# Kernel tuning notes

Measured on AMD Instinct MI355X. Metric: run time of the kernel, lower is better.

## Reference

```python
import jax, jax.numpy as jnp
import numpy as np

B, C_IN, FH, TW = 64, 8, 128, 128
FBINS, A, M_ARR, M_SRC = 257, 360, 4, 2
EPS = 1e-6


def _conv2d(x, w):
    return jax.lax.conv_general_dilated(x, w, (1, 1), 'SAME', dimension_numbers=('NCHW', 'OIHW', 'NCHW'))


def _bn(x, g, b, m, v):
    sh = (1, -1, 1, 1)
    return (x - m.reshape(sh)) * jax.lax.rsqrt(v.reshape(sh) + 1e-5) * g.reshape(sh) + b.reshape(sh)


def _pool2(x):
    b_, c, h, w = x.shape
    return x.reshape(b_, c, h // 2, 2, w // 2, 2).max(axis=(3, 5))


def _block(x, w, g, b, m, v):
    return _pool2(jax.nn.relu(_bn(_conv2d(x, w), g, b, m, v)))


def _conv1d(x, w, b):
    return jax.lax.conv_general_dilated(x, w, (1,), 'SAME', dimension_numbers=('NCH', 'OIH', 'NCH')) + b[None, :, None]


def setup_inputs() -> dict:
    ks = jax.random.split(jax.random.key(0), 16)
    r = lambda i, shp, s=1.0: jax.random.normal(ks[i], shp, dtype=jnp.float32) * s
    d = {
        'X': r(0, (B, C_IN, FH, TW)),
        'sv_real': r(1, (B, FBINS, A, M_ARR)),
        'sv_imag': r(2, (B, FBINS, A, M_ARR)),
        'correlation': jnp.zeros((1,), jnp.float32),
        'conv1_w': r(3, (64, C_IN, 3, 3), 0.1),
        'conv2_w': r(4, (64, 64, 3, 3), 0.04),
        'conv3_w': r(5, (64, 64, 3, 3), 0.04),
        'conv4_w': r(6, (FBINS, 64, 3, 3), 0.04),
        'fc_w': r(7, (32, 64), 0.1),
        'fc_b': jnp.zeros((32,), jnp.float32),
        'convs2_w': r(8, (FBINS, FBINS, 3), 0.02),
        'convs2_b': jnp.zeros((FBINS,), jnp.float32),
        'convs1_w': r(9, (1, FBINS, 3), 0.03),
        'convs1_b': jnp.zeros((1,), jnp.float32),
        'ca_w1': r(10, (16, FBINS), 0.06),
        'ca_w2': r(11, (FBINS, 16), 0.2),
    }
    for i, c in [(1, 64), (2, 64), (3, 64), (4, FBINS)]:
        d[f'bn{i}_g'] = jnp.ones((c,), jnp.float32)
        d[f'bn{i}_b'] = jnp.zeros((c,), jnp.float32)
        d[f'bn{i}_m'] = jnp.zeros((c,), jnp.float32)
        d[f'bn{i}_v'] = jnp.ones((c,), jnp.float32)
    return d


def reference(X, sv_real, sv_imag, correlation,
              conv1_w, bn1_g, bn1_b, bn1_m, bn1_v,
              conv2_w, bn2_g, bn2_b, bn2_m, bn2_v,
              conv3_w, bn3_g, bn3_b, bn3_m, bn3_v,
              conv4_w, bn4_g, bn4_b, bn4_m, bn4_v,
              fc_w, fc_b, convs2_w, convs2_b, convs1_w, convs1_b,
              ca_w1, ca_w2):
    b_ = X.shape[0]
    # CNN encoder: (B,8,128,128) -> (B,257,8,8)
    z = _block(X, conv1_w, bn1_g, bn1_b, bn1_m, bn1_v)
    z = _block(z, conv2_w, bn2_g, bn2_b, bn2_m, bn2_v)
    z = _block(z, conv3_w, bn3_g, bn3_b, bn3_m, bn3_v)
    z = _block(z, conv4_w, bn4_g, bn4_b, bn4_m, bn4_v)
    z = z.reshape(b_, FBINS, -1) @ fc_w.T + fc_b            # (B,257,32)
    z = z.reshape(b_, FBINS, C_IN // 2, C_IN)               # (B,257,4,8)
    Rz = jax.lax.complex(z[..., :M_ARR], z[..., M_ARR:])    # (B,257,4,4)
    # hermitianize + diagonal loading
    Rz = 0.5 * (Rz + jnp.conj(jnp.swapaxes(Rz, -1, -2)))
    Rz = Rz + 1e-5 * jnp.eye(M_ARR, dtype=Rz.dtype)
    _, evecs = jnp.linalg.eigh(Rz)                          # ascending eigenvalues
    Un = evecs[..., ::-1][..., M_SRC:]                      # noise subspace (B,F,4,2)
    UnUnH = Un @ jnp.conj(jnp.swapaxes(Un, -1, -2))         # (B,F,4,4)
    svc = jnp.conj(jax.lax.complex(sv_real, sv_imag))       # (B,F,A,4)
    # faithful to torch code: denom[a] = sum_{m,n} conj(sv[a,m]) UnUnH[m,n] conj(sv[a,n])
    denom = jnp.real(jnp.einsum('bfam,bfmn,bfan->bfa', svc, UnUnH, svc))
    spectrum = 1.0 / jnp.maximum(denom, EPS)                # (B,257,360)
    spectrum = jax.nn.leaky_relu(_conv1d(spectrum, convs2_w, convs2_b), 0.1)
    # channel attention over the 257 freq channels
    y = spectrum.mean(-1)                                   # (B,257)
    att = jax.nn.sigmoid(jax.nn.relu(y @ ca_w1.T) @ ca_w2.T)
    spectrum = spectrum * att[:, :, None]
    spectrum = jax.nn.sigmoid(_conv1d(spectrum, convs1_w, convs1_b))[:, 0, :]  # (B,360)
    # soft-argmax over top-5 peaks
    angles = jnp.linspace(0.0, 360.0, A + 1)[:-1]
    vals, idx = jax.lax.top_k(spectrum, 5)
    wts = jax.nn.softmax(20.0 * vals, axis=-1)
    doa = (wts * angles[idx]).sum(-1)[:, None]              # (B,1)
    return doa, spectrum
```

## Files before the change

kernel.cpp:

```cpp
#include <hip/hip_runtime.h>

typedef unsigned short u16;
typedef unsigned int u32;
typedef short short8 __attribute__((ext_vector_type(8)));
typedef float f32x4 __attribute__((ext_vector_type(4)));

#define NB 64
#define NFB 257
#define NANG 360

__device__ __forceinline__ u16 f2bf(float x) {
    u32 u = __float_as_uint(x);
    u = (u + 0x7fffu + ((u >> 16) & 1u)) >> 16;
    return (u16)u;
}
__device__ __forceinline__ float bf2f(u16 h) { return __uint_as_float(((u32)h) << 16); }

__global__ __launch_bounds__(256) void bnprep(
    const float* g1, const float* b1, const float* m1, const float* v1,
    const float* g2, const float* b2, const float* m2, const float* v2,
    const float* g3, const float* b3, const float* m3, const float* v3,
    const float* g4, const float* b4, const float* m4, const float* v4,
    float* out)
{
    int L = blockIdx.x;
    const float* gs[4] = {g1, g2, g3, g4};
    const float* bs[4] = {b1, b2, b3, b4};
    const float* ms[4] = {m1, m2, m3, m4};
    const float* vs[4] = {v1, v2, v3, v4};
    int n = (L == 3) ? 257 : 64;
    float* sc = out + L * 1024;
    float* bi = sc + 512;
    for (int i = threadIdx.x; i < n; i += 256) {
        float s = gs[L][i] * rsqrtf(vs[L][i] + 1e-5f);
        sc[i] = s;
        bi[i] = bs[L][i] - ms[L][i] * s;
    }
}

__global__ __launch_bounds__(256) void bpack(
    const float* __restrict__ w, u16* __restrict__ Bp,
    int CREAL, int OCREAL, int NT, int KCC, int NFTOT)
{
    int i = blockIdx.x * 256 + threadIdx.x;
    int total = NT * KCC * 2 * NFTOT * 64;
    if (i >= total) return;
    int lane = i & 63;
    int t = i >> 6;
    int nf = t % NFTOT;
    int th = t / NFTOT;
    int h = th & 1;
    int chunk = th >> 1;
    int s = chunk / KCC, kc = chunk % KCC;
    int n = nf * 16 + (lane & 15);
    int k0 = kc * 32 + (lane >> 4) * 8;
    u16 o8[8];
    #pragma unroll
    for (int e = 0; e < 8; ++e) {
        int k = k0 + e;
        float v = 0.f;
        if (k < CREAL && n < OCREAL) v = w[((size_t)n * CREAL + k) * NT + s];
        u16 hh = f2bf(v);
        o8[e] = (h == 0) ? hh : f2bf(v - bf2f(hh));
    }
    u16* d = Bp + (size_t)i * 8;
    #pragma unroll
    for (int e = 0; e < 8; ++e) d[e] = o8[e];
}

__global__ __launch_bounds__(256) void bpack1(const float* __restrict__ w, u16* __restrict__ Bp)
{
    int i = blockIdx.x * 256 + threadIdx.x;
    if (i >= 3 * 2 * 4 * 64) return;
    int lane = i & 63;
    int t = i >> 6;
    int nf = t % 4;
    int th = t / 4;
    int h = th & 1;
    int ky = th >> 1;
    int n = nf * 16 + (lane & 15);
    int q = lane >> 4;
    u16 o8[8];
    #pragma unroll
    for (int e = 0; e < 8; ++e) {
        float v = (q < 3) ? w[((size_t)(n * 8 + e) * 3 + ky) * 3 + q] : 0.f;
        u16 hh = f2bf(v);
        o8[e] = (h == 0) ? hh : f2bf(v - bf2f(hh));
    }
    u16* d = Bp + (size_t)i * 8;
    #pragma unroll
    for (int e = 0; e < 8; ++e) d[e] = o8[e];
}

__global__ __launch_bounds__(256) void xpack_kernel(
    const float* __restrict__ X, u16* __restrict__ hi, u16* __restrict__ lo)
{
    __shared__ float Xs[8][132];
    int bid = blockIdx.x;
    int prow = bid % 130;
    int b = bid / 130;
    bool inr = (prow >= 1 && prow <= 128);
    for (int i = threadIdx.x; i < 8 * 130; i += 256) {
        int c = i / 130, pcol = i % 130;
        float v = 0.f;
        if (inr && pcol >= 1 && pcol <= 128)
            v = X[(((size_t)b * 8 + c) * 128 + (prow - 1)) * 128 + (pcol - 1)];
        Xs[c][pcol] = v;
    }
    __syncthreads();
    for (int p = threadIdx.x; p < 130; p += 256) {
        short8 h8, l8;
        #pragma unroll
        for (int c = 0; c < 8; ++c) {
            float f = Xs[c][p];
            u16 hh = f2bf(f);
            h8[c] = (short)hh;
            l8[c] = (short)f2bf(f - bf2f(hh));
        }
        size_t o = (((size_t)b * 130 + prow) * 130 + p) * 8;
        *(short8*)(hi + o) = h8;
        *(short8*)(lo + o) = l8;
    }
}

__global__ __launch_bounds__(256) void zpad(
    u16* hi, u16* lo, int Bn, int Hp, int Wp, int Cb, int doCols)
{
    int perB = 2 * Wp + (doCols ? 2 * (Hp - 2) : 0);
    long total = (long)Bn * perB * Cb;
    for (long idx = blockIdx.x * 256L + threadIdx.x; idx < total; idx += (long)gridDim.x * 256) {
        int c = (int)(idx % Cb);
        long t = idx / Cb;
        int p = (int)(t % perB);
        int b = (int)(t / perB);
        int row, col;
        if (p < Wp) { row = 0; col = p; }
        else if (p < 2 * Wp) { row = Hp - 1; col = p - Wp; }
        else { int pp = p - 2 * Wp; row = 1 + (pp >> 1); col = (pp & 1) ? (Wp - 1) : 0; }
        size_t o = (((size_t)b * Hp + row) * Wp + col) * Cb + c;
        hi[o] = 0;
        lo[o] = 0;
    }
}

__global__ __launch_bounds__(256) void conv_c1(
    const u16* __restrict__ Ahi, const u16* __restrict__ Alo,
    const u16* __restrict__ Bp,
    const float* __restrict__ esc, const float* __restrict__ ebi,
    u16* __restrict__ Ohi, u16* __restrict__ Olo)
{
    constexpr int Wst = 130, Hp = 130;
    constexpr int SROWS = 5;
    constexpr int SPIX = SROWS * Wst;
    constexpr int STAGEB = SPIX * 16;
    __shared__ __align__(16) char sm[2 * STAGEB];

    int bid = blockIdx.x;
    int ytile = bid % 64;
    int b = bid / 64;
    int y0 = ytile * 2;
    int tid = threadIdx.x;
    int wv = tid >> 6;
    int l = tid & 63;
    int r = l & 15, q = l >> 4;

    for (int pix = tid; pix < SPIX; pix += 256) {
        int prow = y0 + pix / Wst, pcol = pix % Wst;
        uint4 vh = {0, 0, 0, 0}, vl = {0, 0, 0, 0};
        if (prow < Hp) {
            size_t g = (((size_t)b * Hp + prow) * Wst + pcol) * 16;
            vh = *(const uint4*)((const char*)Ahi + g);
            vl = *(const uint4*)((const char*)Alo + g);
        }
        *(uint4*)(sm + pix * 16) = vh;
        *(uint4*)(sm + STAGEB + pix * 16) = vl;
    }
    __syncthreads();

    f32x4 acc[4][4] = {};

    #pragma unroll
    for (int ky = 0; ky < 3; ++ky) {
        short8 bh[4], bl[4];
        #pragma unroll
        for (int ni = 0; ni < 4; ++ni) {
            const u16* bt = Bp + ((size_t)(ky * 2) * 4 + ni) * 512 + l * 8;
            bh[ni] = *(const short8*)bt;
            bl[ni] = *(const short8*)(bt + 4 * 512);
        }
        short8 ah[4], al[4];
        #pragma unroll
        for (int mi = 0; mi < 4; ++mi) {
            int pf = wv * 2 + (mi >> 1);
            int y = mi & 1;
            int p = (y + ky) * Wst + pf * 16 + r + q;
            ah[mi] = *(const short8*)(sm + p * 16);
            al[mi] = *(const short8*)(sm + STAGEB + p * 16);
        }
        #pragma unroll
        for (int ni = 0; ni < 4; ++ni)
            #pragma unroll
            for (int mi = 0; mi < 4; ++mi) {
                acc[mi][ni] = __builtin_amdgcn_mfma_f32_16x16x32_bf16(ah[mi], bh[ni], acc[mi][ni], 0, 0, 0);
                acc[mi][ni] = __builtin_amdgcn_mfma_f32_16x16x32_bf16(ah[mi], bl[ni], acc[mi][ni], 0, 0, 0);
                acc[mi][ni] = __builtin_amdgcn_mfma_f32_16x16x32_bf16(al[mi], bh[ni], acc[mi][ni], 0, 0, 0);
            }
    }

    #pragma unroll
    for (int ni = 0; ni < 4; ++ni) {
        int oc = ni * 16 + r;
        float sc0 = esc[oc], bi0 = ebi[oc];
        #pragma unroll
        for (int pi = 0; pi < 2; ++pi) {
            int pf = wv * 2 + pi;
            #pragma unroll
            for (int k = 0; k < 2; ++k) {
                float m = -3.4e38f;
                #pragma unroll
                for (int dmi = 0; dmi < 2; ++dmi)
                    #pragma unroll
                    for (int dj = 0; dj < 2; ++dj)
                        m = fmaxf(m, fmaf(acc[2 * pi + dmi][ni][2 * k + dj], sc0, bi0));
                m = fmaxf(m, 0.f);
                int x2 = pf * 8 + q * 2 + k;
                size_t o = (((size_t)b * 66 + (y0 / 2 + 1)) * 66 + (x2 + 1)) * 64 + oc;
                u16 hh = f2bf(m);
                Ohi[o] = hh;
                Olo[o] = f2bf(m - bf2f(hh));
            }
        }
    }
}

template<int H, int W, int OC, int R, int NF, int MFW, int OUTMODE, int NFTOT>
__global__ __launch_bounds__(256) void conv_gemm(
    const u16* __restrict__ Ahi, const u16* __restrict__ Alo,
    const u16* __restrict__ Bp,
    const float* __restrict__ esc, const float* __restrict__ ebi,
    u16* __restrict__ Ohi, u16* __restrict__ Olo, float* __restrict__ Of)
{
    constexpr int Wst = W + 2, Hp = H + 2;
    constexpr int SROWS = R + 2;
    constexpr int SPIX = SROWS * Wst;
    constexpr int XF = W / 16;
    constexpr int STAGEB = SPIX * 64;
    constexpr int HT = H / R;
    __shared__ __align__(16) char sm[2 * STAGEB];

    int bid = blockIdx.x;
    int ytile = bid % HT;
    int b = bid / HT;
    int tid = threadIdx.x;
    int wv = tid >> 6;
    int l = tid & 63;
    int r = l & 15, q = l >> 4;
    int y0 = ytile * R;
    int nfg0 = blockIdx.y * NF;

    f32x4 acc[MFW][NF] = {};
    short8 Bh[2][NF], Bl[2][NF];

    auto loadB = [&](int buf, int chunk) {
        #pragma unroll
        for (int ni = 0; ni < NF; ++ni) {
            const u16* bt = Bp + ((size_t)(chunk * 2) * NFTOT + nfg0 + ni) * 512 + l * 8;
            Bh[buf][ni] = *(const short8*)bt;
            Bl[buf][ni] = *(const short8*)(bt + (size_t)NFTOT * 512);
        }
    };
    loadB(0, 0);

    #pragma unroll
    for (int cs = 0; cs < 2; ++cs) {
        __syncthreads();
        for (int i = tid; i < SPIX * 4; i += 256) {
            int pix = i >> 2, sub = i & 3;
            int prow = y0 + pix / Wst, pcol = pix % Wst;
            uint4 vh = {0, 0, 0, 0}, vl = {0, 0, 0, 0};
            if (prow < Hp) {
                size_t g = (((size_t)b * Hp + prow) * Wst + pcol) * 128 + cs * 64 + sub * 16;
                vh = *(const uint4*)((const char*)Ahi + g);
                vl = *(const uint4*)((const char*)Alo + g);
            }
            int dst = (pix << 6) + ((sub ^ ((pix >> 1) & 3)) << 4);
            *(uint4*)(sm + dst) = vh;
            *(uint4*)(sm + STAGEB + dst) = vl;
        }
        __syncthreads();

        #pragma unroll
        for (int s = 0; s < 9; ++s) {
            int cur = (cs * 9 + s) & 1;
            if (s < 8) loadB(cur ^ 1, (s + 1) * 2 + cs);
            else if (cs == 0) loadB(cur ^ 1, 1);
            int ky = s / 3, kx = s % 3;
            short8 ah[MFW], al[MFW];
            #pragma unroll
            for (int mi = 0; mi < MFW; ++mi) {
                int pf = wv * (MFW / 2) + (mi >> 1);
                int y = (pf / XF) * 2 + (mi & 1);
                int xf = pf % XF;
                int p = (y + ky) * Wst + xf * 16 + kx + r;
                int off = (p << 6) + ((q ^ ((p >> 1) & 3)) << 4);
                ah[mi] = *(const short8*)(sm + off);
                al[mi] = *(const short8*)(sm + STAGEB + off);
            }
            #pragma unroll
            for (int ni = 0; ni < NF; ++ni)
                #pragma unroll
                for (int mi = 0; mi < MFW; ++mi) {
                    acc[mi][ni] = __builtin_amdgcn_mfma_f32_16x16x32_bf16(ah[mi], Bh[cur][ni], acc[mi][ni], 0, 0, 0);
                    acc[mi][ni] = __builtin_amdgcn_mfma_f32_16x16x32_bf16(ah[mi], Bl[cur][ni], acc[mi][ni], 0, 0, 0);
                    acc[mi][ni] = __builtin_amdgcn_mfma_f32_16x16x32_bf16(al[mi], Bh[cur][ni], acc[mi][ni], 0, 0, 0);
                }
        }
    }

    #pragma unroll
    for (int ni = 0; ni < NF; ++ni) {
        int oc = (nfg0 + ni) * 16 + r;
        float sc0 = esc[oc], bi0 = ebi[oc];
        #pragma unroll
        for (int pi = 0; pi < MFW / 2; ++pi) {
            int pf = wv * (MFW / 2) + pi;
            int y2 = y0 / 2 + pf / XF;
            int xb = (pf % XF) * 8 + q * 2;
            #pragma unroll
            for (int k = 0; k < 2; ++k) {
                float m = -3.4e38f;
                #pragma unroll
                for (int dmi = 0; dmi < 2; ++dmi)
                    #pragma unroll
                    for (int dj = 0; dj < 2; ++dj)
                        m = fmaxf(m, fmaf(acc[2 * pi + dmi][ni][2 * k + dj], sc0, bi0));
                m = fmaxf(m, 0.f);
                int x2 = xb + k;
                if (OUTMODE == 0) {
                    size_t o = (((size_t)b * (H / 2 + 2) + y2 + 1) * (W / 2 + 2) + (x2 + 1)) * 64 + oc;
                    u16 hh = f2bf(m);
                    Ohi[o] = hh;
                    Olo[o] = f2bf(m - bf2f(hh));
                } else {
                    if (oc < OC)
                        Of[(((size_t)b * (H / 2) + y2) * (W / 2) + x2) * (size_t)OC + oc] = m;
                }
            }
        }
    }
}

__global__ __launch_bounds__(512) void convs2_gemm(
    const u16* __restrict__ Ahi, const u16* __restrict__ Alo,
    const u16* __restrict__ Bp, const float* __restrict__ bia,
    float* __restrict__ sp2)
{
    constexpr int SPIX = 386;
    constexpr int STAGEB = SPIX * 64;
    __shared__ __align__(16) char sm[2 * STAGEB];

    int b = blockIdx.x;
    int nt = blockIdx.y;
    int tid = threadIdx.x;
    int wv = tid >> 6;
    int l = tid & 63;
    int r = l & 15, q = l >> 4;

    f32x4 acc[3][3] = {};
    short8 Bh[2][3], Bl[2][3];

    auto loadB = [&](int buf, int chunk) {
        #pragma unroll
        for (int ni = 0; ni < 3; ++ni) {
            const u16* bt = Bp + ((size_t)(chunk * 2) * 18 + nt * 3 + ni) * 512 + l * 8;
            Bh[buf][ni] = *(const short8*)bt;
            Bl[buf][ni] = *(const short8*)(bt + 18 * 512);
        }
    };
    loadB(0, 0);

    #pragma unroll
    for (int cs = 0; cs < 9; ++cs) {
        __syncthreads();
        for (int i = tid; i < SPIX * 4; i += 512) {
            int pix = i >> 2, sub = i & 3;
            uint4 vh = {0, 0, 0, 0}, vl = {0, 0, 0, 0};
            if (pix < 362) {
                size_t g = ((size_t)b * 362 + pix) * 576 + (size_t)cs * 64 + (size_t)sub * 16;
                vh = *(const uint4*)((const char*)Ahi + g);
                vl = *(const uint4*)((const char*)Alo + g);
            }
            int dst = (pix << 6) + ((sub ^ ((pix >> 1) & 3)) << 4);
            *(uint4*)(sm + dst) = vh;
            *(uint4*)(sm + STAGEB + dst) = vl;
        }
        __syncthreads();

        #pragma unroll
        for (int ky = 0; ky < 3; ++ky) {
            int cur = (cs * 3 + ky) & 1;
            if (ky < 2) loadB(cur ^ 1, (ky + 1) * 9 + cs);
            else if (cs < 8) loadB(cur ^ 1, cs + 1);
            #pragma unroll
            for (int mi = 0; mi < 3; ++mi) {
                int p = (wv * 3 + mi) * 16 + r + ky;
                int off = (p << 6) + ((q ^ ((p >> 1) & 3)) << 4);
                short8 ah = *(const short8*)(sm + off);
                short8 al = *(const short8*)(sm + STAGEB + off);
                #pragma unroll
                for (int ni = 0; ni < 3; ++ni) {
                    acc[mi][ni] = __builtin_amdgcn_mfma_f32_16x16x32_bf16(ah, Bh[cur][ni], acc[mi][ni], 0, 0, 0);
                    acc[mi][ni] = __builtin_amdgcn_mfma_f32_16x16x32_bf16(ah, Bl[cur][ni], acc[mi][ni], 0, 0, 0);
                    acc[mi][ni] = __builtin_amdgcn_mfma_f32_16x16x32_bf16(al, Bh[cur][ni], acc[mi][ni], 0, 0, 0);
                }
            }
        }
    }

    #pragma unroll
    for (int ni = 0; ni < 3; ++ni) {
        int n = (nt * 3 + ni) * 16 + r;
        if (n >= NFB) continue;
        float bi0 = bia[n];
        #pragma unroll
        for (int mi = 0; mi < 3; ++mi) {
            int t0 = (wv * 3 + mi) * 16 + q * 4;
            #pragma unroll
            for (int j = 0; j < 4; ++j) {
                int t = t0 + j;
                if (t < NANG) {
                    float v = acc[mi][ni][j] + bi0;
                    sp2[((size_t)b * NANG + t) * NFB + n] = (v >= 0.f) ? v : 0.1f * v;
                }
            }
        }
    }
}

__global__ __launch_bounds__(256) void fc_kernel(
    const float* __restrict__ z, const float* __restrict__ fw,
    const float* __restrict__ fb, float* __restrict__ zfc)
{
    int bid = blockIdx.x;
    int ftile = bid % 33;
    int b = bid / 33;
    int j = threadIdx.x & 31;
    int f = ftile * 8 + (threadIdx.x >> 5);
    if (f >= 257) return;
    const float* zb = z + (size_t)b * 16448;
    float a = fb[j];
    #pragma unroll 8
    for (int s = 0; s < 64; ++s) a = fmaf(zb[s * 257 + f], fw[j * 64 + s], a);
    zfc[((size_t)b * 257 + f) * 32 + j] = a;
}

__global__ __launch_bounds__(64) void eigh_kernel(const float* __restrict__ z, double* __restrict__ rp)
{
    int idx = blockIdx.x * 64 + threadIdx.x;
    if (idx >= NB * NFB) return;
    const float* zr = z + (size_t)idx * 32;
    double Ar[4][4], Ai[4][4], Vr[4][4], Vi[4][4];
    #pragma unroll
    for (int m = 0; m < 4; ++m)
        #pragma unroll
        for (int n = 0; n < 4; ++n) {
            Ar[m][n] = 0.5 * ((double)zr[m * 8 + n] + (double)zr[n * 8 + m]);
            Ai[m][n] = 0.5 * ((double)zr[m * 8 + n + 4] - (double)zr[n * 8 + m + 4]);
            Vr[m][n] = (m == n) ? 1.0 : 0.0;
            Vi[m][n] = 0.0;
        }
    #pragma unroll
    for (int m = 0; m < 4; ++m) Ar[m][m] += 1e-5;

    for (int sweep = 0; sweep < 8; ++sweep) {
        #pragma unroll
        for (int p = 0; p < 3; ++p)
            #pragma unroll
            for (int qq = p + 1; qq < 4; ++qq) {
                double apr = Ar[p][qq], api = Ai[p][qq];
                double rmod = sqrt(apr * apr + api * api);
                if (rmod < 1e-300) continue;
                double cph = apr / rmod, sph = api / rmod;
                double tau = (Ar[qq][qq] - Ar[p][p]) / (2.0 * rmod);
                double t = (tau >= 0.0) ? (-1.0 / (tau + sqrt(1.0 + tau * tau)))
                                        : (1.0 / (-tau + sqrt(1.0 + tau * tau)));
                double c = 1.0 / sqrt(1.0 + t * t);
                double s = t * c;
                double wr = s * cph, wi = s * sph;
                #pragma unroll
                for (int i = 0; i < 4; ++i) {
                    double xr = Ar[i][p], xi = Ai[i][p];
                    double yr = Ar[i][qq], yi = Ai[i][qq];
                    Ar[i][p] = c * xr + (wr * yr + wi * yi);
                    Ai[i][p] = c * xi + (wr * yi - wi * yr);
                    Ar[i][qq] = c * yr - (wr * xr - wi * xi);
                    Ai[i][qq] = c * yi - (wr * xi + wi * xr);
                }
                #pragma unroll
                for (int i = 0; i < 4; ++i) {
                    double xr = Ar[p][i], xi = Ai[p][i];
                    double yr = Ar[qq][i], yi = Ai[qq][i];
                    Ar[p][i] = c * xr + (wr * yr - wi * yi);
                    Ai[p][i] = c * xi + (wr * yi + wi * yr);
                    Ar[qq][i] = c * yr - (wr * xr + wi * xi);
                    Ai[qq][i] = c * yi - (wr * xi - wi * xr);
                }
                #pragma unroll
                for (int i = 0; i < 4; ++i) {
                    double xr = Vr[i][p], xi = Vi[i][p];
                    double yr = Vr[i][qq], yi = Vi[i][qq];
                    Vr[i][p] = c * xr + (wr * yr + wi * yi);
                    Vi[i][p] = c * xi + (wr * yi - wi * yr);
                    Vr[i][qq] = c * yr - (wr * xr - wi * xi);
                    Vi[i][qq] = c * yi - (wr * xi + wi * xr);
                }
            }
    }
    double ev[4] = {Ar[0][0], Ar[1][1], Ar[2][2], Ar[3][3]};
    int i0 = 0;
    #pragma unroll
    for (int k = 1; k < 4; ++k) if (ev[k] < ev[i0]) i0 = k;
    int i1 = (i0 == 0) ? 1 : 0;
    #pragma unroll
    for (int k = 0; k < 4; ++k) if (k != i0 && ev[k] < ev[i1]) i1 = k;
    double* o = rp + (size_t)idx * 16;
    #pragma unroll
    for (int m = 0; m < 4; ++m)
        #pragma unroll
        for (int n = 0; n < 4; ++n)
            o[m * 4 + n] = Vr[m][i0] * Vr[n][i0] + Vi[m][i0] * Vi[n][i0]
                         + Vr[m][i1] * Vr[n][i1] + Vi[m][i1] * Vi[n][i1];
}

__global__ __launch_bounds__(256) void music_kernel(
    const float4* __restrict__ svr, const float4* __restrict__ svi,
    const double* __restrict__ rp, u16* __restrict__ muhi, u16* __restrict__ mulo)
{
    __shared__ double P[32][16];
    __shared__ float T[32][33];
    int bid = blockIdx.x;
    int at = bid % 12; bid /= 12;
    int ft = bid % 9;
    int b = bid / 9;
    int f0 = ft * 32, a0 = at * 32;
    int tid = threadIdx.x;
    for (int i = tid; i < 32 * 16; i += 256) {
        int fi = i >> 4, j = i & 15;
        int f = f0 + fi;
        P[fi][j] = (f < 257) ? rp[((size_t)b * 257 + f) * 16 + j] : 0.0;
    }
    __syncthreads();
    int asub = tid & 31, fsub = tid >> 5;
    int a = a0 + asub;
    #pragma unroll
    for (int k2 = 0; k2 < 4; ++k2) {
        int fl = fsub + 8 * k2;
        int f = f0 + fl;
        float val = 0.f;
        if (a < 360 && f < 257) {
            float4 u = svr[((size_t)b * 257 + f) * 360 + a];
            float4 w = svi[((size_t)b * 257 + f) * 360 + a];
            const double* Pf = P[fl];
            double ua[4] = {u.x, u.y, u.z, u.w};
            double wa[4] = {w.x, w.y, w.z, w.w};
            double qa = 0.0, qb = 0.0;
            #pragma unroll
            for (int m = 0; m < 4; ++m)
                #pragma unroll
                for (int n = 0; n < 4; ++n) {
                    double pmn = Pf[m * 4 + n];
                    qa += pmn * ua[m] * ua[n];
                    qb += pmn * wa[m] * wa[n];
                }
            double den = qa - qb;
            val = (float)(1.0 / fmax(den, 1e-6));
        }
        T[asub][fl] = val;
    }
    __syncthreads();
    #pragma unroll
    for (int p = 0; p < 4; ++p) {
        int row = p * 8 + (tid >> 5);
        int fc = tid & 31;
        int a2 = a0 + row;
        if (a2 < 360) {
            float v = T[row][fc];
            size_t o = (((size_t)b * 362) + a2 + 1) * 288 + f0 + fc;
            u16 hh = f2bf(v);
            muhi[o] = hh;
            mulo[o] = f2bf(v - bf2f(hh));
        }
    }
}

__global__ __launch_bounds__(256) void attn_partial(const float* __restrict__ sp2, float* __restrict__ part)
{
    int bid = blockIdx.x;
    int ch = bid % 6;
    int b = bid / 6;
    int t0 = ch * 60;
    for (int f = threadIdx.x; f < 257; f += 256) {
        float s = 0.f;
        for (int t = 0; t < 60; ++t) s += sp2[((size_t)b * 360 + t0 + t) * 257 + f];
        part[((size_t)b * 6 + ch) * 257 + f] = s;
    }
}

__global__ __launch_bounds__(256) void attn_finish(
    const float* __restrict__ part, const float* __restrict__ w1,
    const float* __restrict__ w2, float* __restrict__ att)
{
    __shared__ float ys[257];
    __shared__ float hs[16];
    int b = blockIdx.x;
    int tid = threadIdx.x;
    for (int f = tid; f < 257; f += 256) {
        float s = 0.f;
        #pragma unroll
        for (int c = 0; c < 6; ++c) s += part[((size_t)b * 6 + c) * 257 + f];
        ys[f] = s * (1.0f / 360.0f);
    }
    __syncthreads();
    if (tid < 16) {
        float h = 0.f;
        for (int c = 0; c < 257; ++c) h = fmaf(ys[c], w1[(size_t)tid * 257 + c], h);
        hs[tid] = fmaxf(h, 0.f);
    }
    __syncthreads();
    for (int o = tid; o < 257; o += 256) {
        float a = 0.f;
        #pragma unroll
        for (int j = 0; j < 16; ++j) a = fmaf(hs[j], w2[(size_t)o * 16 + j], a);
        att[(size_t)b * 257 + o] = 1.0f / (1.0f + expf(-a));
    }
}

__global__ __launch_bounds__(256) void convs1_kernel(
    const float* __restrict__ sp2, const float* __restrict__ att,
    const float* __restrict__ w, const float* __restrict__ bb,
    float* __restrict__ outS)
{
    int bid = blockIdx.x;
    int tt = bid % 90;
    int b = bid / 90;
    int wv = threadIdx.x >> 6, l = threadIdx.x & 63;
    int t = tt * 4 + wv;
    float s = 0.f;
    for (int f = l; f < 257; f += 64) {
        float av = att[(size_t)b * 257 + f];
        float w0 = w[f * 3] * av, w1 = w[f * 3 + 1] * av, w2 = w[f * 3 + 2] * av;
        const float* col = sp2 + (size_t)b * 360 * 257 + f;
        if (t > 0)   s = fmaf(w0, col[(size_t)(t - 1) * 257], s);
        s = fmaf(w1, col[(size_t)t * 257], s);
        if (t < 359) s = fmaf(w2, col[(size_t)(t + 1) * 257], s);
    }
    #pragma unroll
    for (int off = 32; off > 0; off >>= 1) s += __shfl_down(s, off, 64);
    if (l == 0) outS[(size_t)b * 360 + t] = 1.0f / (1.0f + expf(-(s + bb[0])));
}

__global__ __launch_bounds__(64) void doa_kernel(const float* __restrict__ spec, float* __restrict__ doa)
{
    int b = blockIdx.x;
    int l = threadIdx.x;
    const float* s = spec + (size_t)b * NANG;
    float v[6];
    #pragma unroll
    for (int j = 0; j < 6; ++j) {
        int idx = l + 64 * j;
        v[j] = (idx < NANG) ? s[idx] : -3.4e38f;
    }
    float wvv[5]; int wii[5];
    #pragma unroll
    for (int k = 0; k < 5; ++k) {
        float bv = v[0]; int bj = 0;
        #pragma unroll
        for (int j = 1; j < 6; ++j)
            if (v[j] > bv) { bv = v[j]; bj = j; }
        int bi = l + 64 * bj;
        #pragma unroll
        for (int off = 1; off < 64; off <<= 1) {
            float ov = __shfl_xor(bv, off, 64);
            int oi = __shfl_xor(bi, off, 64);
            if (ov > bv || (ov == bv && oi < bi)) { bv = ov; bi = oi; }
        }
        wvv[k] = bv; wii[k] = bi;
        if ((bi & 63) == l) {
            int j = bi >> 6;
            #pragma unroll
            for (int jj = 0; jj < 6; ++jj)
                if (jj == j) v[jj] = -3.4e38f;
        }
    }
    if (l == 0) {
        float m = wvv[0];
        float wsum = 0.f, asum = 0.f;
        #pragma unroll
        for (int k = 0; k < 5; ++k) {
            float e = expf(20.0f * (wvv[k] - m));
            wsum += e;
            asum += e * (float)wii[k];
        }
        doa[b] = asum / wsum;
    }
}

extern "C" void kernel_launch(void* const* d_in, const int* in_sizes, int n_in,
                              void* d_out, int out_size, void* d_ws, size_t ws_size,
                              hipStream_t stream)
{
    const float* X    = (const float*)d_in[0];
    const float* svr  = (const float*)d_in[1];
    const float* svi  = (const float*)d_in[2];
    const float* c1w  = (const float*)d_in[4];
    const float* c2w  = (const float*)d_in[5];
    const float* c3w  = (const float*)d_in[6];
    const float* c4w  = (const float*)d_in[7];
    const float* fcw  = (const float*)d_in[8];
    const float* fcb  = (const float*)d_in[9];
    const float* s2w  = (const float*)d_in[10];
    const float* s2b  = (const float*)d_in[11];
    const float* s1w  = (const float*)d_in[12];
    const float* s1b  = (const float*)d_in[13];
    const float* caw1 = (const float*)d_in[14];
    const float* caw2 = (const float*)d_in[15];
    const float* bn1g = (const float*)d_in[16]; const float* bn1b = (const float*)d_in[17];
    const float* bn1m = (const float*)d_in[18]; const float* bn1v = (const float*)d_in[19];
    const float* bn2g = (const float*)d_in[20]; const float* bn2b = (const float*)d_in[21];
    const float* bn2m = (const float*)d_in[22]; const float* bn2v = (const float*)d_in[23];
    const float* bn3g = (const float*)d_in[24]; const float* bn3b = (const float*)d_in[25];
    const float* bn3m = (const float*)d_in[26]; const float* bn3v = (const float*)d_in[27];
    const float* bn4g = (const float*)d_in[28]; const float* bn4b = (const float*)d_in[29];
    const float* bn4m = (const float*)d_in[30]; const float* bn4v = (const float*)d_in[31];

    char* wsb = (char*)d_ws;
    u16* xp_hi = (u16*)(wsb + 0);
    u16* xp_lo = (u16*)(wsb + 17305600);
    u16* c3_hi = (u16*)(wsb + 0);
    u16* c3_lo = (u16*)(wsb + 9469952);
    u16* mu_hi = (u16*)(wsb + 0);
    u16* mu_lo = (u16*)(wsb + 13344768);
    const size_t Bb = 34611200;
    u16*   c2_hi = (u16*)(wsb + Bb);
    u16*   c2_lo = (u16*)(wsb + Bb + 35684352);
    float*  zbuf = (float*)(wsb + Bb);
    float*  zfc  = (float*)(wsb + Bb + 4210688);
    double* rp   = (double*)(wsb + Bb + 6316032);
    float*  sp2  = (float*)(wsb + Bb + 8421376);
    float*  part = (float*)(wsb + Bb + 32106496);
    float*  att  = (float*)(wsb + Bb + 32501248);
    const size_t Cb = Bb + 71368704;
    u16* c4_hi = (u16*)(wsb + Cb);
    u16* c4_lo = (u16*)(wsb + Cb + 2654208);
    u16* bp1 = (u16*)(wsb + Cb + 5308416);
    u16* bp2 = (u16*)(wsb + Cb + 5382144);
    u16* bp3 = (u16*)(wsb + Cb + 5529600);
    u16* bp4 = (u16*)(wsb + Cb + 5677056);
    u16* bp5 = (u16*)(wsb + Cb + 6414336);
    float* bns = (float*)(wsb + Cb + 7409664);

    float* outD = (float*)d_out;
    float* outS = (float*)d_out + 64;

    bnprep<<<4, 256, 0, stream>>>(bn1g, bn1b, bn1m, bn1v, bn2g, bn2b, bn2m, bn2v,
                                  bn3g, bn3b, bn3m, bn3v, bn4g, bn4b, bn4m, bn4v, bns);
    bpack1<<<6, 256, 0, stream>>>(c1w, bp1);
    bpack<<<36, 256, 0, stream>>>(c2w, bp2, 64, 64, 9, 2, 4);
    bpack<<<36, 256, 0, stream>>>(c3w, bp3, 64, 64, 9, 2, 4);
    bpack<<<180, 256, 0, stream>>>(c4w, bp4, 64, 257, 9, 2, 20);
    bpack<<<243, 256, 0, stream>>>(s2w, bp5, 257, 257, 3, 9, 18);
    xpack_kernel<<<64 * 130, 256, 0, stream>>>(X, xp_hi, xp_lo);
    zpad<<<4161, 256, 0, stream>>>(c2_hi, c2_lo, 64, 66, 66, 64, 1);
    zpad<<<1088, 256, 0, stream>>>(c4_hi, c4_lo, 64, 18, 18, 64, 1);

    conv_c1<<<64 * 64, 256, 0, stream>>>(xp_hi, xp_lo, bp1, bns, bns + 512, c2_hi, c2_lo);
    zpad<<<2112, 256, 0, stream>>>(c3_hi, c3_lo, 64, 34, 34, 64, 1);
    conv_gemm<64, 64, 64, 2, 4, 2, 0, 4>
        <<<dim3(64 * 32, 1), 256, 0, stream>>>(c2_hi, c2_lo, bp2, bns + 1024, bns + 1536, c3_hi, c3_lo, nullptr);
    conv_gemm<32, 32, 64, 4, 4, 2, 0, 4>
        <<<dim3(64 * 8, 1), 256, 0, stream>>>(c3_hi, c3_lo, bp3, bns + 2048, bns + 2560, c4_hi, c4_lo, nullptr);
    zpad<<<144, 256, 0, stream>>>(mu_hi, mu_lo, 64, 362, 1, 288, 0);
    conv_gemm<16, 16, 257, 8, 4, 2, 1, 20>
        <<<dim3(64 * 2, 5), 256, 0, stream>>>(c4_hi, c4_lo, bp4, bns + 3072, bns + 3584, nullptr, nullptr, zbuf);

    fc_kernel<<<64 * 33, 256, 0, stream>>>(zbuf, fcw, fcb, zfc);
    eigh_kernel<<<NFB, 64, 0, stream>>>(zfc, rp);
    music_kernel<<<64 * 108, 256, 0, stream>>>((const float4*)svr, (const float4*)svi, rp, mu_hi, mu_lo);
    convs2_gemm<<<dim3(64, 6), 512, 0, stream>>>(mu_hi, mu_lo, bp5, s2b, sp2);

    attn_partial<<<64 * 6, 256, 0, stream>>>(sp2, part);
    attn_finish<<<64, 256, 0, stream>>>(part, caw1, caw2, att);
    convs1_kernel<<<64 * 90, 256, 0, stream>>>(sp2, att, s1w, s1b, outS);
    doa_kernel<<<64, 64, 0, stream>>>(outS, outD);
}
```

Measured before the change: 428.6 us.

## Interleave bf16 hi/lo split planes into one buffer and split convs2 tiles

Replaces the separate hi and lo bf16 activation buffers with one interleaved layout, placing the hi and lo halves of each 32-channel chunk next to each other. Every staging load now fetches a single contiguous 128-byte line per pixel chunk instead of two loads from distant buffers. The LDS swizzle changes to match, and lo is read at off^64. convs2_gemm is also split into two time tiles per batch with 256-thread blocks, which raises block count and lowers LDS use per block. The catch is that the zero-padding and indexing logic has to stay in step with the new interleaved layout.

```diff
diff --git a/kernel.cpp b/kernel.cpp
--- a/kernel.cpp
+++ b/kernel.cpp
@@ -15,6 +15,7 @@
     return (u16)u;
 }
 __device__ __forceinline__ float bf2f(u16 h) { return __uint_as_float(((u32)h) << 16); }
+
 
 __global__ __launch_bounds__(256) void bnprep(
     const float* g1, const float* b1, const float* m1, const float* v1,
@@ -93,7 +94,7 @@
 }
 
 __global__ __launch_bounds__(256) void xpack_kernel(
-    const float* __restrict__ X, u16* __restrict__ hi, u16* __restrict__ lo)
+    const float* __restrict__ X, u16* __restrict__ xp)
 {
     __shared__ float Xs[8][132];
     int bid = blockIdx.x;
@@ -117,43 +118,39 @@
             h8[c] = (short)hh;
             l8[c] = (short)f2bf(f - bf2f(hh));
         }
-        size_t o = (((size_t)b * 130 + prow) * 130 + p) * 8;
-        *(short8*)(hi + o) = h8;
-        *(short8*)(lo + o) = l8;
+        size_t o = (((size_t)b * 130 + prow) * 130 + p) * 16;
+        *(short8*)(xp + o) = h8;
+        *(short8*)(xp + o + 8) = l8;
     }
 }
 
 __global__ __launch_bounds__(256) void zpad(
-    u16* hi, u16* lo, int Bn, int Hp, int Wp, int Cb, int doCols)
+    u32* buf, int Bn, int Hp, int Wp, int wpp, int doCols)
 {
     int perB = 2 * Wp + (doCols ? 2 * (Hp - 2) : 0);
-    long total = (long)Bn * perB * Cb;
+    long total = (long)Bn * perB * wpp;
     for (long idx = blockIdx.x * 256L + threadIdx.x; idx < total; idx += (long)gridDim.x * 256) {
-        int c = (int)(idx % Cb);
-        long t = idx / Cb;
+        int w = (int)(idx % wpp);
+        long t = idx / wpp;
         int p = (int)(t % perB);
         int b = (int)(t / perB);
         int row, col;
         if (p < Wp) { row = 0; col = p; }
         else if (p < 2 * Wp) { row = Hp - 1; col = p - Wp; }
         else { int pp = p - 2 * Wp; row = 1 + (pp >> 1); col = (pp & 1) ? (Wp - 1) : 0; }
-        size_t o = (((size_t)b * Hp + row) * Wp + col) * Cb + c;
-        hi[o] = 0;
-        lo[o] = 0;
+        buf[(((size_t)b * Hp + row) * Wp + col) * (size_t)wpp + w] = 0;
     }
 }
 
 __global__ __launch_bounds__(256) void conv_c1(
-    const u16* __restrict__ Ahi, const u16* __restrict__ Alo,
-    const u16* __restrict__ Bp,
+    const u16* __restrict__ A, const u16* __restrict__ Bp,
     const float* __restrict__ esc, const float* __restrict__ ebi,
-    u16* __restrict__ Ohi, u16* __restrict__ Olo)
+    u16* __restrict__ O)
 {
     constexpr int Wst = 130, Hp = 130;
     constexpr int SROWS = 5;
     constexpr int SPIX = SROWS * Wst;
-    constexpr int STAGEB = SPIX * 16;
-    __shared__ __align__(16) char sm[2 * STAGEB];
+    __shared__ __align__(16) char sm[SPIX * 48];
 
     int bid = blockIdx.x;
     int ytile = bid % 64;
@@ -164,16 +161,13 @@
     int l = tid & 63;
     int r = l & 15, q = l >> 4;
 
-    for (int pix = tid; pix < SPIX; pix += 256) {
+    for (int i = tid; i < SPIX * 2; i += 256) {
+        int pix = i >> 1, sub = i & 1;
         int prow = y0 + pix / Wst, pcol = pix % Wst;
-        uint4 vh = {0, 0, 0, 0}, vl = {0, 0, 0, 0};
-        if (prow < Hp) {
-            size_t g = (((size_t)b * Hp + prow) * Wst + pcol) * 16;
-            vh = *(const uint4*)((const char*)Ahi + g);
-            vl = *(const uint4*)((const char*)Alo + g);
-        }
-        *(uint4*)(sm + pix * 16) = vh;
-        *(uint4*)(sm + STAGEB + pix * 16) = vl;
+        uint4 v = {0, 0, 0, 0};
+        if (prow < Hp)
+            v = *(const uint4*)(A + (((size_t)b * Hp + prow) * Wst + pcol) * 16 + sub * 8);
+        *(uint4*)(sm + pix * 48 + sub * 16) = v;
     }
     __syncthreads();
 
@@ -194,8 +188,8 @@
             int pf = wv * 2 + (mi >> 1);
             int y = mi & 1;
             int p = (y + ky) * Wst + pf * 16 + r + q;
-            ah[mi] = *(const short8*)(sm + p * 16);
-            al[mi] = *(const short8*)(sm + STAGEB + p * 16);
+            ah[mi] = *(const short8*)(sm + p * 48);
+            al[mi] = *(const short8*)(sm + p * 48 + 16);
         }
         #pragma unroll
         for (int ni = 0; ni < 4; ++ni)
@@ -224,10 +218,11 @@
                         m = fmaxf(m, fmaf(acc[2 * pi + dmi][ni][2 * k + dj], sc0, bi0));
                 m = fmaxf(m, 0.f);
                 int x2 = pf * 8 + q * 2 + k;
-                size_t o = (((size_t)b * 66 + (y0 / 2 + 1)) * 66 + (x2 + 1)) * 64 + oc;
+                size_t base = (((size_t)b * 66 + (y0 / 2 + 1)) * 66 + (x2 + 1)) * 128;
+                u16* d = O + base + ((oc >> 5) << 6) + (oc & 31);
                 u16 hh = f2bf(m);
-                Ohi[o] = hh;
-                Olo[o] = f2bf(m - bf2f(hh));
+                d[0] = hh;
+                d[32] = f2bf(m - bf2f(hh));
             }
         }
     }
@@ -235,18 +230,16 @@
 
 template<int H, int W, int OC, int R, int NF, int MFW, int OUTMODE, int NFTOT>
 __global__ __launch_bounds__(256) void conv_gemm(
-    const u16* __restrict__ Ahi, const u16* __restrict__ Alo,
-    const u16* __restrict__ Bp,
+    const u16* __restrict__ A, const u16* __restrict__ Bp,
     const float* __restrict__ esc, const float* __restrict__ ebi,
-    u16* __restrict__ Ohi, u16* __restrict__ Olo, float* __restrict__ Of)
+    u16* __restrict__ O, float* __restrict__ Of)
 {
     constexpr int Wst = W + 2, Hp = H + 2;
     constexpr int SROWS = R + 2;
     constexpr int SPIX = SROWS * Wst;
     constexpr int XF = W / 16;
-    constexpr int STAGEB = SPIX * 64;
     constexpr int HT = H / R;
-    __shared__ __align__(16) char sm[2 * STAGEB];
+    __shared__ __align__(16) char sm[SPIX * 128];
 
     int bid = blockIdx.x;
     int ytile = bid % HT;
@@ -274,18 +267,13 @@
     #pragma unroll
     for (int cs = 0; cs < 2; ++cs) {
         __syncthreads();
-        for (int i = tid; i < SPIX * 4; i += 256) {
-            int pix = i >> 2, sub = i & 3;
+        for (int i = tid; i < SPIX * 8; i += 256) {
+            int pix = i >> 3, sub = i & 7;
             int prow = y0 + pix / Wst, pcol = pix % Wst;
-            uint4 vh = {0, 0, 0, 0}, vl = {0, 0, 0, 0};
-            if (prow < Hp) {
-                size_t g = (((size_t)b * Hp + prow) * Wst + pcol) * 128 + cs * 64 + sub * 16;
-                vh = *(const uint4*)((const char*)Ahi + g);
-                vl = *(const uint4*)((const char*)Alo + g);
-            }
-            int dst = (pix << 6) + ((sub ^ ((pix >> 1) & 3)) << 4);
-            *(uint4*)(sm + dst) = vh;
-            *(uint4*)(sm + STAGEB + dst) = vl;
+            uint4 v = {0, 0, 0, 0};
+            if (prow < Hp)
+                v = *(const uint4*)(A + (((size_t)b * Hp + prow) * Wst + pcol) * 128 + cs * 64 + sub * 8);
+            *(uint4*)(sm + pix * 128 + ((sub ^ (pix & 7)) << 4)) = v;
         }
         __syncthreads();
 
@@ -302,9 +290,9 @@
                 int y = (pf / XF) * 2 + (mi & 1);
                 int xf = pf % XF;
                 int p = (y + ky) * Wst + xf * 16 + kx + r;
-                int off = (p << 6) + ((q ^ ((p >> 1) & 3)) << 4);
+                int off = p * 128 + ((q ^ (p & 7)) << 4);
                 ah[mi] = *(const short8*)(sm + off);
-                al[mi] = *(const short8*)(sm + STAGEB + off);
+                al[mi] = *(const short8*)(sm + (off ^ 64));
             }
             #pragma unroll
             for (int ni = 0; ni < NF; ++ni)
@@ -337,10 +325,11 @@
                 m = fmaxf(m, 0.f);
                 int x2 = xb + k;
                 if (OUTMODE == 0) {
-                    size_t o = (((size_t)b * (H / 2 + 2) + y2 + 1) * (W / 2 + 2) + (x2 + 1)) * 64 + oc;
+                    size_t base = (((size_t)b * (H / 2 + 2) + y2 + 1) * (W / 2 + 2) + (x2 + 1)) * 128;
+                    u16* d = O + base + ((oc >> 5) << 6) + (oc & 31);
                     u16 hh = f2bf(m);
-                    Ohi[o] = hh;
-                    Olo[o] = f2bf(m - bf2f(hh));
+                    d[0] = hh;
+                    d[32] = f2bf(m - bf2f(hh));
                 } else {
                     if (oc < OC)
                         Of[(((size_t)b * (H / 2) + y2) * (W / 2) + x2) * (size_t)OC + oc] = m;
@@ -350,17 +339,18 @@
     }
 }
 
-__global__ __launch_bounds__(512) void convs2_gemm(
-    const u16* __restrict__ Ahi, const u16* __restrict__ Alo,
-    const u16* __restrict__ Bp, const float* __restrict__ bia,
-    float* __restrict__ sp2)
-{
-    constexpr int SPIX = 386;
-    constexpr int STAGEB = SPIX * 64;
-    __shared__ __align__(16) char sm[2 * STAGEB];
-
-    int b = blockIdx.x;
+__global__ __launch_bounds__(256) void convs2_gemm(
+    const u16* __restrict__ A, const u16* __restrict__ Bp,
+    const float* __restrict__ bia, float* __restrict__ sp2)
+{
+    constexpr int SPIX = 194;
+    __shared__ __align__(16) char sm[SPIX * 128];
+
+    int bid = blockIdx.x;
+    int tt = bid & 1;
+    int b = bid >> 1;
     int nt = blockIdx.y;
+    int t0 = tt * 192;
     int tid = threadIdx.x;
     int wv = tid >> 6;
     int l = tid & 63;
@@ -382,17 +372,13 @@
     #pragma unroll
     for (int cs = 0; cs < 9; ++cs) {
         __syncthreads();
-        for (int i = tid; i < SPIX * 4; i += 512) {
-            int pix = i >> 2, sub = i & 3;
-            uint4 vh = {0, 0, 0, 0}, vl = {0, 0, 0, 0};
-            if (pix < 362) {
-                size_t g = ((size_t)b * 362 + pix) * 576 + (size_t)cs * 64 + (size_t)sub * 16;
-                vh = *(const uint4*)((const char*)Ahi + g);
-                vl = *(const uint4*)((const char*)Alo + g);
-            }
-            int dst = (pix << 6) + ((sub ^ ((pix >> 1) & 3)) << 4);
-            *(uint4*)(sm + dst) = vh;
-            *(uint4*)(sm + STAGEB + dst) = vl;
+        for (int i = tid; i < SPIX * 8; i += 256) {
+            int pix = i >> 3, sub = i & 7;
+            int gp = t0 + pix;
+            uint4 v = {0, 0, 0, 0};
+            if (gp < 362)
+                v = *(const uint4*)(A + ((size_t)b * 362 + gp) * 576 + cs * 64 + sub * 8);
+            *(uint4*)(sm + pix * 128 + ((sub ^ (pix & 7)) << 4)) = v;
         }
         __syncthreads();
 
@@ -404,9 +390,9 @@
             #pragma unroll
             for (int mi = 0; mi < 3; ++mi) {
                 int p = (wv * 3 + mi) * 16 + r + ky;
-                int off = (p << 6) + ((q ^ ((p >> 1) & 3)) << 4);
+                int off = p * 128 + ((q ^ (p & 7)) << 4);
                 short8 ah = *(const short8*)(sm + off);
-                short8 al = *(const short8*)(sm + STAGEB + off);
+                short8 al = *(const short8*)(sm + (off ^ 64));
                 #pragma unroll
                 for (int ni = 0; ni < 3; ++ni) {
                     acc[mi][ni] = __builtin_amdgcn_mfma_f32_16x16x32_bf16(ah, Bh[cur][ni], acc[mi][ni], 0, 0, 0);
@@ -424,10 +410,10 @@
         float bi0 = bia[n];
         #pragma unroll
         for (int mi = 0; mi < 3; ++mi) {
-            int t0 = (wv * 3 + mi) * 16 + q * 4;
+            int tb = t0 + (wv * 3 + mi) * 16 + q * 4;
             #pragma unroll
             for (int j = 0; j < 4; ++j) {
-                int t = t0 + j;
+                int t = tb + j;
                 if (t < NANG) {
                     float v = acc[mi][ni][j] + bi0;
                     sp2[((size_t)b * NANG + t) * NFB + n] = (v >= 0.f) ? v : 0.1f * v;
@@ -534,7 +520,7 @@
 
 __global__ __launch_bounds__(256) void music_kernel(
     const float4* __restrict__ svr, const float4* __restrict__ svi,
-    const double* __restrict__ rp, u16* __restrict__ muhi, u16* __restrict__ mulo)
+    const double* __restrict__ rp, u16* __restrict__ mu)
 {
     __shared__ double P[32][16];
     __shared__ float T[32][33];
@@ -578,6 +564,7 @@
         T[asub][fl] = val;
     }
     __syncthreads();
+    int sec0 = f0 >> 5;
     #pragma unroll
     for (int p = 0; p < 4; ++p) {
         int row = p * 8 + (tid >> 5);
@@ -585,10 +572,10 @@
         int a2 = a0 + row;
         if (a2 < 360) {
             float v = T[row][fc];
-            size_t o = (((size_t)b * 362) + a2 + 1) * 288 + f0 + fc;
+            u16* d = mu + ((size_t)b * 362 + a2 + 1) * 576 + (size_t)sec0 * 64 + fc;
             u16 hh = f2bf(v);
-            muhi[o] = hh;
-            mulo[o] = f2bf(v - bf2f(hh));
+            d[0] = hh;
+            d[32] = f2bf(v - bf2f(hh));
         }
     }
 }
@@ -734,15 +721,11 @@
     const float* bn4m = (const float*)d_in[30]; const float* bn4v = (const float*)d_in[31];
 
     char* wsb = (char*)d_ws;
-    u16* xp_hi = (u16*)(wsb + 0);
-    u16* xp_lo = (u16*)(wsb + 17305600);
-    u16* c3_hi = (u16*)(wsb + 0);
-    u16* c3_lo = (u16*)(wsb + 9469952);
-    u16* mu_hi = (u16*)(wsb + 0);
-    u16* mu_lo = (u16*)(wsb + 13344768);
+    u16* xp = (u16*)(wsb + 0);
+    u16* c3 = (u16*)(wsb + 0);
+    u16* mu = (u16*)(wsb + 0);
     const size_t Bb = 34611200;
-    u16*   c2_hi = (u16*)(wsb + Bb);
-    u16*   c2_lo = (u16*)(wsb + Bb + 35684352);
+    u16*   c2  = (u16*)(wsb + Bb);
     float*  zbuf = (float*)(wsb + Bb);
     float*  zfc  = (float*)(wsb + Bb + 4210688);
     double* rp   = (double*)(wsb + Bb + 6316032);
@@ -750,8 +733,7 @@
     float*  part = (float*)(wsb + Bb + 32106496);
     float*  att  = (float*)(wsb + Bb + 32501248);
     const size_t Cb = Bb + 71368704;
-    u16* c4_hi = (u16*)(wsb + Cb);
-    u16* c4_lo = (u16*)(wsb + Cb + 2654208);
+    u16* c4  = (u16*)(wsb + Cb);
     u16* bp1 = (u16*)(wsb + Cb + 5308416);
     u16* bp2 = (u16*)(wsb + Cb + 5382144);
     u16* bp3 = (u16*)(wsb + Cb + 5529600);
@@ -769,24 +751,24 @@
     bpack<<<36, 256, 0, stream>>>(c3w, bp3, 64, 64, 9, 2, 4);
     bpack<<<180, 256, 0, stream>>>(c4w, bp4, 64, 257, 9, 2, 20);
     bpack<<<243, 256, 0, stream>>>(s2w, bp5, 257, 257, 3, 9, 18);
-    xpack_kernel<<<64 * 130, 256, 0, stream>>>(X, xp_hi, xp_lo);
-    zpad<<<4161, 256, 0, stream>>>(c2_hi, c2_lo, 64, 66, 66, 64, 1);
-    zpad<<<1088, 256, 0, stream>>>(c4_hi, c4_lo, 64, 18, 18, 64, 1);
-
-    conv_c1<<<64 * 64, 256, 0, stream>>>(xp_hi, xp_lo, bp1, bns, bns + 512, c2_hi, c2_lo);
-    zpad<<<2112, 256, 0, stream>>>(c3_hi, c3_lo, 64, 34, 34, 64, 1);
+    xpack_kernel<<<64 * 130, 256, 0, stream>>>(X, xp);
+    zpad<<<4160, 256, 0, stream>>>((u32*)c2, 64, 66, 66, 64, 1);
+    zpad<<<1088, 256, 0, stream>>>((u32*)c4, 64, 18, 18, 64, 1);
+
+    conv_c1<<<64 * 64, 256, 0, stream>>>(xp, bp1, bns, bns + 512, c2);
+    zpad<<<2112, 256, 0, stream>>>((u32*)c3, 64, 34, 34, 64, 1);
     conv_gemm<64, 64, 64, 2, 4, 2, 0, 4>
-        <<<dim3(64 * 32, 1), 256, 0, stream>>>(c2_hi, c2_lo, bp2, bns + 1024, bns + 1536, c3_hi, c3_lo, nullptr);
+        <<<dim3(64 * 32, 1), 256, 0, stream>>>(c2, bp2, bns + 1024, bns + 1536, c3, nullptr);
     conv_gemm<32, 32, 64, 4, 4, 2, 0, 4>
-        <<<dim3(64 * 8, 1), 256, 0, stream>>>(c3_hi, c3_lo, bp3, bns + 2048, bns + 2560, c4_hi, c4_lo, nullptr);
-    zpad<<<144, 256, 0, stream>>>(mu_hi, mu_lo, 64, 362, 1, 288, 0);
+        <<<dim3(64 * 8, 1), 256, 0, stream>>>(c3, bp3, bns + 2048, bns + 2560, c4, nullptr);
+    zpad<<<144, 256, 0, stream>>>((u32*)mu, 64, 362, 1, 288, 0);
     conv_gemm<16, 16, 257, 8, 4, 2, 1, 20>
-        <<<dim3(64 * 2, 5), 256, 0, stream>>>(c4_hi, c4_lo, bp4, bns + 3072, bns + 3584, nullptr, nullptr, zbuf);
+        <<<dim3(64 * 2, 5), 256, 0, stream>>>(c4, bp4, bns + 3072, bns + 3584, nullptr, zbuf);
 
     fc_kernel<<<64 * 33, 256, 0, stream>>>(zbuf, fcw, fcb, zfc);
     eigh_kernel<<<NFB, 64, 0, stream>>>(zfc, rp);
-    music_kernel<<<64 * 108, 256, 0, stream>>>((const float4*)svr, (const float4*)svi, rp, mu_hi, mu_lo);
-    convs2_gemm<<<dim3(64, 6), 512, 0, stream>>>(mu_hi, mu_lo, bp5, s2b, sp2);
+    music_kernel<<<64 * 108, 256, 0, stream>>>((const float4*)svr, (const float4*)svi, rp, mu);
+    convs2_gemm<<<dim3(64 * 2, 6), 256, 0, stream>>>(mu, bp5, s2b, sp2);
 
     attn_partial<<<64 * 6, 256, 0, stream>>>(sp2, part);
     attn_finish<<<64, 256, 0, stream>>>(part, caw1, caw2, att);
```

Measured after the change: 442.5 us. +3.2%, slower.
